# Kernel tuning notes

Hardware: AMD Instinct MI355X
Metric: run time of the kernel (lower is better)

Reference implementation:

```python
import jax, jax.numpy as jnp
import numpy as np

N_NODES = 100000
N_EDGES = 1600000
N_QEDGES = 400000
NUM_FEAT = 128
HIDDEN_C = 128
OUT_C = 64
NO_HEADS = 8


def setup_inputs() -> dict:
    key = jax.random.key(0)
    ks = jax.random.split(key, 8)
    x = jax.random.normal(ks[0], (N_NODES, NUM_FEAT), dtype=jnp.float32)
    W1 = jax.random.normal(ks[1], (NUM_FEAT, HIDDEN_C), dtype=jnp.float32) * (1.0 / np.sqrt(NUM_FEAT))
    b1 = jnp.zeros((HIDDEN_C,), dtype=jnp.float32)
    W2 = jax.random.normal(ks[2], (HIDDEN_C, OUT_C * NO_HEADS), dtype=jnp.float32) * (1.0 / np.sqrt(HIDDEN_C))
    b2 = jnp.zeros((OUT_C * NO_HEADS,), dtype=jnp.float32)
    edge_index = jax.random.randint(ks[3], (2, N_EDGES), 0, N_NODES, dtype=jnp.int32)
    q_edge_index = jax.random.randint(ks[4], (2, N_QEDGES), 0, N_NODES, dtype=jnp.int32)
    y = jax.random.randint(ks[5], (N_NODES,), 0, NO_HEADS, dtype=jnp.int32)
    return {"x": x, "W1": W1, "b1": b1, "W2": W2, "b2": b2,
            "edge_index": edge_index, "q_edge_index": q_edge_index, "y": y}


def gcn_conv(x, W, b, src, dst, n):
    """GCNConv: symmetric normalization with implicit self-loops."""
    h = x @ W  # [n, out]
    ones = jnp.ones(src.shape[0], dtype=x.dtype)
    deg = jax.ops.segment_sum(ones, dst, num_segments=n) + 1.0  # self-loop
    dinv = jax.lax.rsqrt(deg)
    norm = dinv[src] * dinv[dst]  # [E]
    agg = jax.ops.segment_sum(h[src] * norm[:, None], dst, num_segments=n)
    agg = agg + h * (dinv * dinv)[:, None]  # self-loop message
    return agg + b


def reference(x, W1, b1, W2, b2, edge_index, q_edge_index, y):
    src, dst = edge_index[0], edge_index[1]
    n = x.shape[0]
    hiddens = jax.nn.relu(gcn_conv(x, W1, b1, src, dst, n))            # [N, H]
    emb = gcn_conv(hiddens, W2, b2, src, dst, n)                        # [N, heads*out]
    emb = emb.reshape(n, NO_HEADS, OUT_C)                               # [N, h, f]
    q_row, q_col = q_edge_index[0], q_edge_index[1]
    preds = jnp.einsum('ehf,ehf->eh', emb[q_row], emb[q_col])           # [Q, h]
    pred_i = jnp.take_along_axis(preds, y[q_row][:, None].astype(jnp.int32), axis=1)[:, 0]
    pred_j = jnp.take_along_axis(preds, y[q_col][:, None].astype(jnp.int32), axis=1)[:, 0]
    pred = (pred_i + pred_j) * 0.5  # multiheads=True branch
    return hiddens, emb, pred_i, pred_j, pred
```

## Files before the change

### kernel.cpp

```cpp
#include <hip/hip_runtime.h>
#include <hip/hip_bf16.h>


#define SCAN_SEG 512

typedef short bf16x8 __attribute__((ext_vector_type(8)));
typedef float f32x4  __attribute__((ext_vector_type(4)));

__device__ __forceinline__ ushort f2bf(float x) {
    return (ushort)(__float_as_uint(x) >> 16);
}
__device__ __forceinline__ float bf2f(ushort h) {
    return __uint_as_float(((unsigned)h) << 16);
}

__global__ void count_kernel(const int* __restrict__ dst, int* __restrict__ cnt, int E) {
    int e = blockIdx.x * blockDim.x + threadIdx.x;
    if (e < E) atomicAdd(&cnt[dst[e]], 1);
}

__global__ __launch_bounds__(256) void blocksum_kernel(const int* __restrict__ cnt,
                                                       int* __restrict__ blocksum, int n) {
    __shared__ int red[4];
    int b = blockIdx.x, t = threadIdx.x;
    int i0 = b * SCAN_SEG + t;
    int s = 0;
    if (i0 < n) s += cnt[i0];
    if (i0 + 256 < n) s += cnt[i0 + 256];
#pragma unroll
    for (int off = 32; off >= 1; off >>= 1) s += __shfl_xor(s, off, 64);
    if ((t & 63) == 0) red[t >> 6] = s;
    __syncthreads();
    if (t == 0) blocksum[b] = red[0] + red[1] + red[2] + red[3];
}

__global__ __launch_bounds__(256) void blockscan_kernel(const int* __restrict__ blocksum,
                                                        int* __restrict__ blockoff, int nb,
                                                        int* __restrict__ row_ptr, int n, int E) {
    __shared__ int s[256];
    int t = threadIdx.x;
    int v = (t < nb) ? blocksum[t] : 0;
    s[t] = v;
    __syncthreads();
    for (int off = 1; off < 256; off <<= 1) {
        int u = (t >= off) ? s[t - off] : 0;
        __syncthreads();
        s[t] += u;
        __syncthreads();
    }
    if (t < nb) blockoff[t] = s[t] - v;
    if (t == 0) row_ptr[n] = E;
}

__global__ __launch_bounds__(256) void csr_ptr_kernel(const int* __restrict__ cnt,
                                                      const int* __restrict__ blockoff,
                                                      int* __restrict__ row_ptr,
                                                      int* __restrict__ cursor,
                                                      float* __restrict__ dinv, int n) {
    __shared__ int s[256];
    int b = blockIdx.x, t = threadIdx.x;
    int i0 = b * SCAN_SEG + 2 * t;
    int c0 = (i0     < n) ? cnt[i0]     : 0;
    int c1 = (i0 + 1 < n) ? cnt[i0 + 1] : 0;
    int pair = c0 + c1;
    s[t] = pair;
    __syncthreads();
    for (int off = 1; off < 256; off <<= 1) {
        int u = (t >= off) ? s[t - off] : 0;
        __syncthreads();
        s[t] += u;
        __syncthreads();
    }
    int excl = s[t] - pair + blockoff[b];
    if (i0 < n) {
        row_ptr[i0] = excl;
        cursor[i0]  = excl;
        dinv[i0]    = rsqrtf((float)(c0 + 1));
    }
    if (i0 + 1 < n) {
        row_ptr[i0 + 1] = excl + c0;
        cursor[i0 + 1]  = excl + c0;
        dinv[i0 + 1]    = rsqrtf((float)(c1 + 1));
    }
}

__global__ void fill_kernel(const int* __restrict__ src, const int* __restrict__ dst,
                            int* __restrict__ cursor, const float* __restrict__ dinv,
                            int2* __restrict__ csr, int E) {
    int e = blockIdx.x * blockDim.x + threadIdx.x;
    if (e < E) {
        int s = src[e], d = dst[e];
        int pos = atomicAdd(&cursor[d], 1);
        csr[pos] = make_int2(s, __float_as_int(dinv[s] * dinv[d]));
    }
}

__global__ __launch_bounds__(256) void wsplit_kernel(const float* __restrict__ W,
                                                     ushort* __restrict__ th,
                                                     ushort* __restrict__ tl, int ncols) {
    int idx = blockIdx.x * 256 + threadIdx.x;
    if (idx >= 128 * ncols) return;
    int col = idx >> 7;
    int k   = idx & 127;
    float v = W[(size_t)k * ncols + col];
    ushort h = f2bf(v);
    th[idx] = h;
    tl[idx] = f2bf(v - bf2f(h));
}

__global__ __launch_bounds__(256) void agg_kernel(const float* __restrict__ feat,
                                                  const int* __restrict__ row_ptr,
                                                  const int2* __restrict__ csr,
                                                  const float* __restrict__ dinv,
                                                  ushort* __restrict__ outh,
                                                  ushort* __restrict__ outl, int n) {
    const int w    = threadIdx.x >> 6;
    const int lane = threadIdx.x & 63;
    const int node = blockIdx.x * 4 + w;
    if (node >= n) return;
    const int g = lane >> 5;
    const int c = lane & 31;

    float di = dinv[node];
    float4 acc = make_float4(0.f, 0.f, 0.f, 0.f);
    if (g == 0) {
        float4 v = ((const float4*)(feat + (size_t)node * 128))[c];
        float s2 = di * di;
        acc.x = v.x * s2; acc.y = v.y * s2; acc.z = v.z * s2; acc.w = v.w * s2;
    }

    int e0 = row_ptr[node], e1 = row_ptr[node + 1];
    int e = e0 + g;
    for (; e + 6 < e1; e += 8) {
        int2 p0 = csr[e],     p1 = csr[e + 2];
        int2 p2 = csr[e + 4], p3 = csr[e + 6];
        float w0 = __int_as_float(p0.y), w1 = __int_as_float(p1.y);
        float w2 = __int_as_float(p2.y), w3 = __int_as_float(p3.y);
        float4 v0 = ((const float4*)(feat + (size_t)p0.x * 128))[c];
        float4 v1 = ((const float4*)(feat + (size_t)p1.x * 128))[c];
        float4 v2 = ((const float4*)(feat + (size_t)p2.x * 128))[c];
        float4 v3 = ((const float4*)(feat + (size_t)p3.x * 128))[c];
        acc.x += v0.x * w0 + v1.x * w1 + v2.x * w2 + v3.x * w3;
        acc.y += v0.y * w0 + v1.y * w1 + v2.y * w2 + v3.y * w3;
        acc.z += v0.z * w0 + v1.z * w1 + v2.z * w2 + v3.z * w3;
        acc.w += v0.w * w0 + v1.w * w1 + v2.w * w2 + v3.w * w3;
    }
    for (; e < e1; e += 2) {
        int2 p0 = csr[e];
        float w0 = __int_as_float(p0.y);
        float4 v0 = ((const float4*)(feat + (size_t)p0.x * 128))[c];
        acc.x += v0.x * w0; acc.y += v0.y * w0; acc.z += v0.z * w0; acc.w += v0.w * w0;
    }

    acc.x += __shfl_xor(acc.x, 32, 64);
    acc.y += __shfl_xor(acc.y, 32, 64);
    acc.z += __shfl_xor(acc.z, 32, 64);
    acc.w += __shfl_xor(acc.w, 32, 64);

    if (g == 0) {
        ushort4 h, l;
        h.x = f2bf(acc.x); l.x = f2bf(acc.x - bf2f(h.x));
        h.y = f2bf(acc.y); l.y = f2bf(acc.y - bf2f(h.y));
        h.z = f2bf(acc.z); l.z = f2bf(acc.z - bf2f(h.z));
        h.w = f2bf(acc.w); l.w = f2bf(acc.w - bf2f(h.w));
        *(ushort4*)(outh + (size_t)node * 128 + c * 4) = h;
        *(ushort4*)(outl + (size_t)node * 128 + c * 4) = l;
    }
}

__global__ __launch_bounds__(256, 2) void gemm_mfma(const ushort* __restrict__ Xh_g,
                                                    const ushort* __restrict__ Xl_g,
                                                    const ushort* __restrict__ Wth_g,
                                                    const ushort* __restrict__ Wtl_g,
                                                    const float* __restrict__ bias,
                                                    float* __restrict__ C,
                                                    int N, int ldw, int do_relu) {
    __shared__ ushort Xh[128 * 64];
    __shared__ ushort Xl[128 * 64];
    __shared__ ushort Wh[128 * 64];
    __shared__ ushort Wl[128 * 64];

    const int tid  = threadIdx.x;
    const int lane = tid & 63;
    const int wv   = tid >> 6;
    const int wr   = wv >> 1;
    const int wc   = wv & 1;
    const int lr   = lane & 15;
    const int lk   = lane >> 4;
    const int row0   = blockIdx.y * 128;
    const int colOff = blockIdx.x * 128;

    f32x4 acc[4][4];
#pragma unroll
    for (int i = 0; i < 4; ++i)
#pragma unroll
        for (int j = 0; j < 4; ++j)
            acc[i][j] = (f32x4){0.f, 0.f, 0.f, 0.f};

    for (int ph = 0; ph < 2; ++ph) {
        if (ph) __syncthreads();

#pragma unroll
        for (int q = 0; q < 4; ++q) {
            int cidx = tid + 256 * q;
            int row  = cidx >> 3;
            int kch  = cidx & 7;
            int gr   = row0 + row; if (gr >= N) gr = N - 1;
            size_t ge = (size_t)gr * 128 + ph * 64 + kch * 8;
            int lb = row * 128 + ((kch * 16) ^ ((row & 7) << 4));
            *(int4*)((char*)Xh + lb) = *(const int4*)(Xh_g + ge);
            *(int4*)((char*)Xl + lb) = *(const int4*)(Xl_g + ge);
        }
#pragma unroll
        for (int q = 0; q < 4; ++q) {
            int cidx = tid + 256 * q;
            int col  = cidx >> 3;
            int kch  = cidx & 7;
            size_t ge = (size_t)(colOff + col) * 128 + ph * 64 + kch * 8;
            int lb = col * 128 + ((kch * 16) ^ ((col & 7) << 4));
            *(int4*)((char*)Wh + lb) = *(const int4*)(Wth_g + ge);
            *(int4*)((char*)Wl + lb) = *(const int4*)(Wtl_g + ge);
        }
        __syncthreads();

#pragma unroll
        for (int kk = 0; kk < 2; ++kk) {
            const int kb2 = (kk * 32 + lk * 8) * 2;
            bf16x8 ah[4], al[4], bh[4], bl[4];
#pragma unroll
            for (int mi = 0; mi < 4; ++mi) {
                int row  = wr * 64 + mi * 16 + lr;
                int byte = row * 128 + (kb2 ^ ((row & 7) << 4));
                ah[mi] = *(const bf16x8*)((const char*)Xh + byte);
                al[mi] = *(const bf16x8*)((const char*)Xl + byte);
            }
#pragma unroll
            for (int ni = 0; ni < 4; ++ni) {
                int col  = wc * 64 + ni * 16 + lr;
                int byte = col * 128 + (kb2 ^ ((col & 7) << 4));
                bh[ni] = *(const bf16x8*)((const char*)Wh + byte);
                bl[ni] = *(const bf16x8*)((const char*)Wl + byte);
            }
#pragma unroll
            for (int mi = 0; mi < 4; ++mi)
#pragma unroll
                for (int ni = 0; ni < 4; ++ni) {
                    acc[mi][ni] = __builtin_amdgcn_mfma_f32_16x16x32_bf16(
                        ah[mi], bh[ni], acc[mi][ni], 0, 0, 0);
                    acc[mi][ni] = __builtin_amdgcn_mfma_f32_16x16x32_bf16(
                        ah[mi], bl[ni], acc[mi][ni], 0, 0, 0);
                    acc[mi][ni] = __builtin_amdgcn_mfma_f32_16x16x32_bf16(
                        al[mi], bh[ni], acc[mi][ni], 0, 0, 0);
                }
        }
    }

#pragma unroll
    for (int ni = 0; ni < 4; ++ni) {
        int col = colOff + wc * 64 + ni * 16 + lr;
        float bv = bias[col];
#pragma unroll
        for (int mi = 0; mi < 4; ++mi) {
            int rbase = row0 + wr * 64 + mi * 16 + (lane >> 4) * 4;
#pragma unroll
            for (int r = 0; r < 4; ++r) {
                int row = rbase + r;
                if (row < N) {
                    float v = acc[mi][ni][r] + bv;
                    if (do_relu) v = fmaxf(v, 0.f);
                    C[(size_t)row * ldw + col] = v;
                }
            }
        }
    }
}

__global__ __launch_bounds__(256) void query_kernel(const float* __restrict__ emb,
                                                    const int* __restrict__ qrow,
                                                    const int* __restrict__ qcol,
                                                    const int* __restrict__ y,
                                                    float* __restrict__ pred_i,
                                                    float* __restrict__ pred_j,
                                                    float* __restrict__ pred, int Q) {
    int wave = (int)((blockIdx.x * 256 + threadIdx.x) >> 6);
    int lane = threadIdx.x & 63;
    if (wave >= Q) return;
    int r = qrow[wave], c = qcol[wave];
    int yr = y[r], yc = y[c];
    int g = lane >> 4;
    int t = lane & 15;
    int node = (g & 1) ? c : r;
    int head = (g >> 1) ? yc : yr;
    const float4* p = (const float4*)(emb + (size_t)node * 512 + head * 64);
    float4 v = p[t];
    float4 o;
    o.x = __shfl_xor(v.x, 16, 64);
    o.y = __shfl_xor(v.y, 16, 64);
    o.z = __shfl_xor(v.z, 16, 64);
    o.w = __shfl_xor(v.w, 16, 64);
    float s = v.x * o.x + v.y * o.y + v.z * o.z + v.w * o.w;
#pragma unroll
    for (int off = 8; off >= 1; off >>= 1) s += __shfl_xor(s, off, 64);
    float other = __shfl_xor(s, 32, 64);
    if (lane == 0) {
        pred_i[wave] = s;
        pred_j[wave] = other;
        pred[wave]   = 0.5f * (s + other);
    }
}

extern "C" void kernel_launch(void* const* d_in, const int* in_sizes, int n_in,
                              void* d_out, int out_size, void* d_ws, size_t ws_size,
                              hipStream_t stream) {
    const float* x   = (const float*)d_in[0];
    const float* W1  = (const float*)d_in[1];
    const float* b1  = (const float*)d_in[2];
    const float* W2  = (const float*)d_in[3];
    const float* b2  = (const float*)d_in[4];
    const int* edge  = (const int*)d_in[5];
    const int* qedge = (const int*)d_in[6];
    const int* y     = (const int*)d_in[7];

    const int N = in_sizes[0] / 128;
    const int E = in_sizes[5] / 2;
    const int Q = in_sizes[6] / 2;

    float* out     = (float*)d_out;
    float* hiddens = out;
    float* emb     = out + (size_t)N * 128;
    float* pred_i  = emb + (size_t)N * 512;
    float* pred_j  = pred_i + Q;
    float* pred    = pred_j + Q;

    char* w = (char*)d_ws;
    auto alloc = [&](size_t bytes) { char* p = w; w += (bytes + 255) & ~(size_t)255; return p; };
    int*    cnt      = (int*)alloc((size_t)N * 4);
    int*    row_ptr  = (int*)alloc((size_t)(N + 1) * 4);
    int*    cursor   = (int*)alloc((size_t)N * 4);
    float*  dinv     = (float*)alloc((size_t)N * 4);
    int2*   csr      = (int2*)alloc((size_t)E * 8);
    int*    blocksum = (int*)alloc(256 * 4);
    int*    blockoff = (int*)alloc(256 * 4);
    ushort* aggh     = (ushort*)alloc((size_t)N * 128 * 2);
    ushort* aggl     = (ushort*)alloc((size_t)N * 128 * 2);
    ushort* w1h      = (ushort*)alloc(128 * 128 * 2);
    ushort* w1l      = (ushort*)alloc(128 * 128 * 2);
    ushort* w2h      = (ushort*)alloc(128 * 512 * 2);
    ushort* w2l      = (ushort*)alloc(128 * 512 * 2);

    const int* esrc = edge;         const int* edst = edge + E;
    const int* qrow = qedge;        const int* qcol = qedge + Q;

    const int nb = (N + SCAN_SEG - 1) / SCAN_SEG;

    hipMemsetAsync(cnt, 0, (size_t)N * 4, stream);
    count_kernel<<<dim3((E + 255) / 256), dim3(256), 0, stream>>>(edst, cnt, E);
    blocksum_kernel<<<dim3(nb), dim3(256), 0, stream>>>(cnt, blocksum, N);
    blockscan_kernel<<<dim3(1), dim3(256), 0, stream>>>(blocksum, blockoff, nb, row_ptr, N, E);
    csr_ptr_kernel<<<dim3(nb), dim3(256), 0, stream>>>(cnt, blockoff, row_ptr, cursor, dinv, N);
    fill_kernel<<<dim3((E + 255) / 256), dim3(256), 0, stream>>>(esrc, edst, cursor, dinv, csr, E);

    wsplit_kernel<<<dim3((128 * 128 + 255) / 256), dim3(256), 0, stream>>>(W1, w1h, w1l, 128);
    wsplit_kernel<<<dim3((128 * 512 + 255) / 256), dim3(256), 0, stream>>>(W2, w2h, w2l, 512);

    const int mblocks = (N + 127) / 128;
    const int ablocks = (N + 3) / 4;

    agg_kernel<<<dim3(ablocks), dim3(256), 0, stream>>>(x, row_ptr, csr, dinv, aggh, aggl, N);
    gemm_mfma<<<dim3(1, mblocks), dim3(256), 0, stream>>>(aggh, aggl, w1h, w1l, b1, hiddens, N, 128, 1);

    agg_kernel<<<dim3(ablocks), dim3(256), 0, stream>>>(hiddens, row_ptr, csr, dinv, aggh, aggl, N);
    gemm_mfma<<<dim3(4, mblocks), dim3(256), 0, stream>>>(aggh, aggl, w2h, w2l, b2, emb, N, 512, 0);

    query_kernel<<<dim3((Q + 3) / 4), dim3(256), 0, stream>>>(emb, qrow, qcol, y, pred_i, pred_j, pred, Q);
}
```

Baseline: 916.2 us.

## Gather fp16 features in aggregation and use fp16 split-weight MFMA GEMM

Converts input features to fp16 once, and has the layer-1 GEMM also write an fp16 copy of hiddens, so both aggregation kernels gather half-width rows instead of fp32 rows. This halves the random-gather traffic that dominates aggregation. The aggregated result is stored as a single fp16 tensor rather than a bf16 hi/lo pair, and the GEMM drops from three MFMAs to two per tile (fp16 activations times hi/lo fp16 weights), freeing LDS so occupancy can rise to 3 blocks. The cost is lower activation precision (fp16 range and mantissa), an extra conversion kernel, and an extra fp16 store in the first GEMM.

New measurement: 813.3 us. 11.2% less time.

```diff
diff --git a/kernel.cpp b/kernel.cpp
--- a/kernel.cpp
+++ b/kernel.cpp
@@ -1,18 +1,13 @@
 #include <hip/hip_runtime.h>
 #include <hip/hip_bf16.h>
+#include <hip/hip_fp16.h>
 
 
 #define SCAN_SEG 512
 
-typedef short bf16x8 __attribute__((ext_vector_type(8)));
-typedef float f32x4  __attribute__((ext_vector_type(4)));
-
-__device__ __forceinline__ ushort f2bf(float x) {
-    return (ushort)(__float_as_uint(x) >> 16);
-}
-__device__ __forceinline__ float bf2f(ushort h) {
-    return __uint_as_float(((unsigned)h) << 16);
-}
+typedef _Float16 f16x8 __attribute__((ext_vector_type(8)));
+typedef _Float16 f16x4 __attribute__((ext_vector_type(4)));
+typedef float    f32x4 __attribute__((ext_vector_type(4)));
 
 __global__ void count_kernel(const int* __restrict__ dst, int* __restrict__ cnt, int E) {
     int e = blockIdx.x * blockDim.x + threadIdx.x;
@@ -95,25 +90,35 @@
     }
 }
 
+__global__ __launch_bounds__(256) void tohalf_kernel(const float* __restrict__ x,
+                                                     _Float16* __restrict__ xh, int n) {
+    int id = blockIdx.x * 256 + threadIdx.x;
+    if (id >= n * 32) return;
+    float4 v = ((const float4*)x)[id];
+    f16x4 h;
+    h[0] = (_Float16)v.x; h[1] = (_Float16)v.y;
+    h[2] = (_Float16)v.z; h[3] = (_Float16)v.w;
+    ((f16x4*)xh)[id] = h;
+}
+
 __global__ __launch_bounds__(256) void wsplit_kernel(const float* __restrict__ W,
-                                                     ushort* __restrict__ th,
-                                                     ushort* __restrict__ tl, int ncols) {
+                                                     _Float16* __restrict__ th,
+                                                     _Float16* __restrict__ tl, int ncols) {
     int idx = blockIdx.x * 256 + threadIdx.x;
     if (idx >= 128 * ncols) return;
     int col = idx >> 7;
     int k   = idx & 127;
     float v = W[(size_t)k * ncols + col];
-    ushort h = f2bf(v);
+    _Float16 h = (_Float16)v;
     th[idx] = h;
-    tl[idx] = f2bf(v - bf2f(h));
-}
-
-__global__ __launch_bounds__(256) void agg_kernel(const float* __restrict__ feat,
+    tl[idx] = (_Float16)(v - (float)h);
+}
+
+__global__ __launch_bounds__(256) void agg_kernel(const _Float16* __restrict__ feat,
                                                   const int* __restrict__ row_ptr,
                                                   const int2* __restrict__ csr,
                                                   const float* __restrict__ dinv,
-                                                  ushort* __restrict__ outh,
-                                                  ushort* __restrict__ outl, int n) {
+                                                  _Float16* __restrict__ outf, int n) {
     const int w    = threadIdx.x >> 6;
     const int lane = threadIdx.x & 63;
     const int node = blockIdx.x * 4 + w;
@@ -124,9 +129,10 @@
     float di = dinv[node];
     float4 acc = make_float4(0.f, 0.f, 0.f, 0.f);
     if (g == 0) {
-        float4 v = ((const float4*)(feat + (size_t)node * 128))[c];
+        f16x4 v = ((const f16x4*)(feat + (size_t)node * 128))[c];
         float s2 = di * di;
-        acc.x = v.x * s2; acc.y = v.y * s2; acc.z = v.z * s2; acc.w = v.w * s2;
+        acc.x = (float)v[0] * s2; acc.y = (float)v[1] * s2;
+        acc.z = (float)v[2] * s2; acc.w = (float)v[3] * s2;
     }
 
     int e0 = row_ptr[node], e1 = row_ptr[node + 1];
@@ -136,20 +142,21 @@
         int2 p2 = csr[e + 4], p3 = csr[e + 6];
         float w0 = __int_as_float(p0.y), w1 = __int_as_float(p1.y);
         float w2 = __int_as_float(p2.y), w3 = __int_as_float(p3.y);
-        float4 v0 = ((const float4*)(feat + (size_t)p0.x * 128))[c];
-        float4 v1 = ((const float4*)(feat + (size_t)p1.x * 128))[c];
-        float4 v2 = ((const float4*)(feat + (size_t)p2.x * 128))[c];
-        float4 v3 = ((const float4*)(feat + (size_t)p3.x * 128))[c];
-        acc.x += v0.x * w0 + v1.x * w1 + v2.x * w2 + v3.x * w3;
-        acc.y += v0.y * w0 + v1.y * w1 + v2.y * w2 + v3.y * w3;
-        acc.z += v0.z * w0 + v1.z * w1 + v2.z * w2 + v3.z * w3;
-        acc.w += v0.w * w0 + v1.w * w1 + v2.w * w2 + v3.w * w3;
+        f16x4 v0 = ((const f16x4*)(feat + (size_t)p0.x * 128))[c];
+        f16x4 v1 = ((const f16x4*)(feat + (size_t)p1.x * 128))[c];
+        f16x4 v2 = ((const f16x4*)(feat + (size_t)p2.x * 128))[c];
+        f16x4 v3 = ((const f16x4*)(feat + (size_t)p3.x * 128))[c];
+        acc.x += (float)v0[0] * w0 + (float)v1[0] * w1 + (float)v2[0] * w2 + (float)v3[0] * w3;
+        acc.y += (float)v0[1] * w0 + (float)v1[1] * w1 + (float)v2[1] * w2 + (float)v3[1] * w3;
+        acc.z += (float)v0[2] * w0 + (float)v1[2] * w1 + (float)v2[2] * w2 + (float)v3[2] * w3;
+        acc.w += (float)v0[3] * w0 + (float)v1[3] * w1 + (float)v2[3] * w2 + (float)v3[3] * w3;
     }
     for (; e < e1; e += 2) {
         int2 p0 = csr[e];
         float w0 = __int_as_float(p0.y);
-        float4 v0 = ((const float4*)(feat + (size_t)p0.x * 128))[c];
-        acc.x += v0.x * w0; acc.y += v0.y * w0; acc.z += v0.z * w0; acc.w += v0.w * w0;
+        f16x4 v0 = ((const f16x4*)(feat + (size_t)p0.x * 128))[c];
+        acc.x += (float)v0[0] * w0; acc.y += (float)v0[1] * w0;
+        acc.z += (float)v0[2] * w0; acc.w += (float)v0[3] * w0;
     }
 
     acc.x += __shfl_xor(acc.x, 32, 64);
@@ -158,27 +165,23 @@
     acc.w += __shfl_xor(acc.w, 32, 64);
 
     if (g == 0) {
-        ushort4 h, l;
-        h.x = f2bf(acc.x); l.x = f2bf(acc.x - bf2f(h.x));
-        h.y = f2bf(acc.y); l.y = f2bf(acc.y - bf2f(h.y));
-        h.z = f2bf(acc.z); l.z = f2bf(acc.z - bf2f(h.z));
-        h.w = f2bf(acc.w); l.w = f2bf(acc.w - bf2f(h.w));
-        *(ushort4*)(outh + (size_t)node * 128 + c * 4) = h;
-        *(ushort4*)(outl + (size_t)node * 128 + c * 4) = l;
-    }
-}
-
-__global__ __launch_bounds__(256, 2) void gemm_mfma(const ushort* __restrict__ Xh_g,
-                                                    const ushort* __restrict__ Xl_g,
-                                                    const ushort* __restrict__ Wth_g,
-                                                    const ushort* __restrict__ Wtl_g,
+        f16x4 o;
+        o[0] = (_Float16)acc.x; o[1] = (_Float16)acc.y;
+        o[2] = (_Float16)acc.z; o[3] = (_Float16)acc.w;
+        ((f16x4*)(outf + (size_t)node * 128))[c] = o;
+    }
+}
+
+__global__ __launch_bounds__(256, 3) void gemm_mfma(const _Float16* __restrict__ X_g,
+                                                    const _Float16* __restrict__ Wth_g,
+                                                    const _Float16* __restrict__ Wtl_g,
                                                     const float* __restrict__ bias,
                                                     float* __restrict__ C,
+                                                    _Float16* __restrict__ tbl,
                                                     int N, int ldw, int do_relu) {
-    __shared__ ushort Xh[128 * 64];
-    __shared__ ushort Xl[128 * 64];
-    __shared__ ushort Wh[128 * 64];
-    __shared__ ushort Wl[128 * 64];
+    __shared__ _Float16 Xs[128 * 64];
+    __shared__ _Float16 Wh[128 * 64];
+    __shared__ _Float16 Wl[128 * 64];
 
     const int tid  = threadIdx.x;
     const int lane = tid & 63;
@@ -208,8 +211,7 @@
             int gr   = row0 + row; if (gr >= N) gr = N - 1;
             size_t ge = (size_t)gr * 128 + ph * 64 + kch * 8;
             int lb = row * 128 + ((kch * 16) ^ ((row & 7) << 4));
-            *(int4*)((char*)Xh + lb) = *(const int4*)(Xh_g + ge);
-            *(int4*)((char*)Xl + lb) = *(const int4*)(Xl_g + ge);
+            *(int4*)((char*)Xs + lb) = *(const int4*)(X_g + ge);
         }
 #pragma unroll
         for (int q = 0; q < 4; ++q) {
@@ -225,32 +227,29 @@
 
 #pragma unroll
         for (int kk = 0; kk < 2; ++kk) {
-            const int kb2 = (kk * 32 + lk * 8) * 2;
-            bf16x8 ah[4], al[4], bh[4], bl[4];
+            const int kb = (kk * 32 + lk * 8) * 2;
+            f16x8 a[4], bh[4], bl[4];
 #pragma unroll
             for (int mi = 0; mi < 4; ++mi) {
                 int row  = wr * 64 + mi * 16 + lr;
-                int byte = row * 128 + (kb2 ^ ((row & 7) << 4));
-                ah[mi] = *(const bf16x8*)((const char*)Xh + byte);
-                al[mi] = *(const bf16x8*)((const char*)Xl + byte);
+                int byte = row * 128 + (kb ^ ((row & 7) << 4));
+                a[mi] = *(const f16x8*)((const char*)Xs + byte);
             }
 #pragma unroll
             for (int ni = 0; ni < 4; ++ni) {
                 int col  = wc * 64 + ni * 16 + lr;
-                int byte = col * 128 + (kb2 ^ ((col & 7) << 4));
-                bh[ni] = *(const bf16x8*)((const char*)Wh + byte);
-                bl[ni] = *(const bf16x8*)((const char*)Wl + byte);
+                int byte = col * 128 + (kb ^ ((col & 7) << 4));
+                bh[ni] = *(const f16x8*)((const char*)Wh + byte);
+                bl[ni] = *(const f16x8*)((const char*)Wl + byte);
             }
 #pragma unroll
             for (int mi = 0; mi < 4; ++mi)
 #pragma unroll
                 for (int ni = 0; ni < 4; ++ni) {
-                    acc[mi][ni] = __builtin_amdgcn_mfma_f32_16x16x32_bf16(
-                        ah[mi], bh[ni], acc[mi][ni], 0, 0, 0);
-                    acc[mi][ni] = __builtin_amdgcn_mfma_f32_16x16x32_bf16(
-                        ah[mi], bl[ni], acc[mi][ni], 0, 0, 0);
-                    acc[mi][ni] = __builtin_amdgcn_mfma_f32_16x16x32_bf16(
-                        al[mi], bh[ni], acc[mi][ni], 0, 0, 0);
+                    acc[mi][ni] = __builtin_amdgcn_mfma_f32_16x16x32_f16(
+                        a[mi], bh[ni], acc[mi][ni], 0, 0, 0);
+                    acc[mi][ni] = __builtin_amdgcn_mfma_f32_16x16x32_f16(
+                        a[mi], bl[ni], acc[mi][ni], 0, 0, 0);
                 }
         }
     }
@@ -269,6 +268,7 @@
                     float v = acc[mi][ni][r] + bv;
                     if (do_relu) v = fmaxf(v, 0.f);
                     C[(size_t)row * ldw + col] = v;
+                    if (tbl) tbl[(size_t)row * 128 + col] = (_Float16)v;
                 }
             }
         }
@@ -334,19 +334,19 @@
 
     char* w = (char*)d_ws;
     auto alloc = [&](size_t bytes) { char* p = w; w += (bytes + 255) & ~(size_t)255; return p; };
-    int*    cnt      = (int*)alloc((size_t)N * 4);
-    int*    row_ptr  = (int*)alloc((size_t)(N + 1) * 4);
-    int*    cursor   = (int*)alloc((size_t)N * 4);
-    float*  dinv     = (float*)alloc((size_t)N * 4);
-    int2*   csr      = (int2*)alloc((size_t)E * 8);
-    int*    blocksum = (int*)alloc(256 * 4);
-    int*    blockoff = (int*)alloc(256 * 4);
-    ushort* aggh     = (ushort*)alloc((size_t)N * 128 * 2);
-    ushort* aggl     = (ushort*)alloc((size_t)N * 128 * 2);
-    ushort* w1h      = (ushort*)alloc(128 * 128 * 2);
-    ushort* w1l      = (ushort*)alloc(128 * 128 * 2);
-    ushort* w2h      = (ushort*)alloc(128 * 512 * 2);
-    ushort* w2l      = (ushort*)alloc(128 * 512 * 2);
+    int*      cnt      = (int*)alloc((size_t)N * 4);
+    int*      row_ptr  = (int*)alloc((size_t)(N + 1) * 4);
+    int*      cursor   = (int*)alloc((size_t)N * 4);
+    float*    dinv     = (float*)alloc((size_t)N * 4);
+    int2*     csr      = (int2*)alloc((size_t)E * 8);
+    int*      blocksum = (int*)alloc(256 * 4);
+    int*      blockoff = (int*)alloc(256 * 4);
+    _Float16* tblh     = (_Float16*)alloc((size_t)N * 128 * 2);
+    _Float16* aggf     = (_Float16*)alloc((size_t)N * 128 * 2);
+    _Float16* w1h      = (_Float16*)alloc(128 * 128 * 2);
+    _Float16* w1l      = (_Float16*)alloc(128 * 128 * 2);
+    _Float16* w2h      = (_Float16*)alloc(128 * 512 * 2);
+    _Float16* w2l      = (_Float16*)alloc(128 * 512 * 2);
 
     const int* esrc = edge;         const int* edst = edge + E;
     const int* qrow = qedge;        const int* qcol = qedge + Q;
@@ -358,6 +358,7 @@
     blocksum_kernel<<<dim3(nb), dim3(256), 0, stream>>>(cnt, blocksum, N);
     blockscan_kernel<<<dim3(1), dim3(256), 0, stream>>>(blocksum, blockoff, nb, row_ptr, N, E);
     csr_ptr_kernel<<<dim3(nb), dim3(256), 0, stream>>>(cnt, blockoff, row_ptr, cursor, dinv, N);
+    tohalf_kernel<<<dim3((N * 32 + 255) / 256), dim3(256), 0, stream>>>(x, tblh, N);
     fill_kernel<<<dim3((E + 255) / 256), dim3(256), 0, stream>>>(esrc, edst, cursor, dinv, csr, E);
 
     wsplit_kernel<<<dim3((128 * 128 + 255) / 256), dim3(256), 0, stream>>>(W1, w1h, w1l, 128);
@@ -366,11 +367,13 @@
     const int mblocks = (N + 127) / 128;
     const int ablocks = (N + 3) / 4;
 
-    agg_kernel<<<dim3(ablocks), dim3(256), 0, stream>>>(x, row_ptr, csr, dinv, aggh, aggl, N);
-    gemm_mfma<<<dim3(1, mblocks), dim3(256), 0, stream>>>(aggh, aggl, w1h, w1l, b1, hiddens, N, 128, 1);
-
-    agg_kernel<<<dim3(ablocks), dim3(256), 0, stream>>>(hiddens, row_ptr, csr, dinv, aggh, aggl, N);
-    gemm_mfma<<<dim3(4, mblocks), dim3(256), 0, stream>>>(aggh, aggl, w2h, w2l, b2, emb, N, 512, 0);
+    agg_kernel<<<dim3(ablocks), dim3(256), 0, stream>>>(tblh, row_ptr, csr, dinv, aggf, N);
+    gemm_mfma<<<dim3(1, mblocks), dim3(256), 0, stream>>>(aggf, w1h, w1l, b1, hiddens,
+                                                          tblh, N, 128, 1);
+
+    agg_kernel<<<dim3(ablocks), dim3(256), 0, stream>>>(tblh, row_ptr, csr, dinv, aggf, N);
+    gemm_mfma<<<dim3(4, mblocks), dim3(256), 0, stream>>>(aggf, w2h, w2l, b2, emb,
+                                                          nullptr, N, 512, 0);
 
     query_kernel<<<dim3((Q + 3) / 4), dim3(256), 0, stream>>>(emb, qrow, qcol, y, pred_i, pred_j, pred, Q);
 }
```
